# Performance work log

Hardware: AMD Instinct MI355X
Metric: run time of the kernel (lower is better)

## Reference

```python
import jax, jax.numpy as jnp
import numpy as np
import math

DIM_IN = 1024
DIM_HIDDEN = 512
NUM_SUBKEYS = 256
TOP_K = 32
NUM_HEADS = 4
BN_EPS = 1e-5


def setup_inputs() -> dict:
    key = jax.random.key(0)
    ks = jax.random.split(key, 6)
    std = 1.0 / math.sqrt(DIM_HIDDEN)
    x = jax.random.normal(ks[0], (4, 256, DIM_IN), dtype=jnp.float32)
    # nn.Linear weight: [out, in] = [dim_hidden*num_heads, dim_in]
    Wq = jax.random.normal(ks[1], (DIM_HIDDEN * NUM_HEADS, DIM_IN), dtype=jnp.float32) / math.sqrt(DIM_IN)
    bn_gamma = jnp.ones((DIM_HIDDEN * NUM_HEADS,), dtype=jnp.float32)
    bn_beta = jnp.zeros((DIM_HIDDEN * NUM_HEADS,), dtype=jnp.float32)
    subkey = DIM_HIDDEN // 2
    keyl = jax.random.uniform(ks[2], (NUM_HEADS, NUM_SUBKEYS, subkey), dtype=jnp.float32, minval=-std, maxval=std)
    keyr = jax.random.uniform(ks[3], (NUM_HEADS, NUM_SUBKEYS, subkey), dtype=jnp.float32, minval=-std, maxval=std)
    value_table = jax.random.normal(ks[4], (NUM_SUBKEYS * NUM_SUBKEYS, DIM_IN), dtype=jnp.float32)
    return {"x": x, "Wq": Wq, "bn_gamma": bn_gamma, "bn_beta": bn_beta,
            "keyl": keyl, "keyr": keyr, "value_table": value_table}


def reference(x, Wq, bn_gamma, bn_beta, keyl, keyr, value_table):
    b, c, _ = x.shape
    k = TOP_K
    subkey = DIM_HIDDEN // 2

    # QueryNetwork: linear (no bias) + BatchNorm1d (training-mode batch stats)
    q = jnp.einsum('bci,oi->bco', x, Wq)                      # [b, c, H*Dh]
    qf = q.reshape(-1, DIM_HIDDEN * NUM_HEADS)
    mean = jnp.mean(qf, axis=0)
    var = jnp.var(qf, axis=0)                                  # biased, as in torch BN forward
    qf = (qf - mean) * jax.lax.rsqrt(var + BN_EPS) * bn_gamma + bn_beta
    query = qf.reshape(b, c, NUM_HEADS, DIM_HIDDEN)

    # ProductKey: dual subkey scoring
    ql, qr = query[..., :subkey], query[..., subkey:]
    scorel = jnp.einsum('bcnq,nkq->bcnk', ql, keyl)            # [b,c,n,num_subkeys]
    scorer = jnp.einsum('bcnq,nkq->bcnk', qr, keyr)
    top_l, idx_l = jax.lax.top_k(scorel, k)                    # [b,c,n,k]
    top_r, idx_r = jax.lax.top_k(scorer, k)

    # Cartesian product of scores: s[i,j] = top_l[i] + top_r[j]
    product_scores = (top_l[..., :, None] + top_r[..., None, :]).reshape(b, c, NUM_HEADS, k * k)
    # NOTE: faithful to original code, idx_r is broadcast along the SAME (left)
    # axis as idx_l (original expands [...,k,1] -> [...,k,k] for both).
    pair_idx = idx_l * NUM_SUBKEYS + idx_r                     # [b,c,n,k]
    product_indices = jnp.broadcast_to(pair_idx[..., :, None], (b, c, NUM_HEADS, k, k)).reshape(b, c, NUM_HEADS, k * k)

    top_scores, top_pos = jax.lax.top_k(product_scores, k)     # [b,c,n,k]
    weights = jax.nn.softmax(top_scores, axis=-1)
    sel_idx = jnp.take_along_axis(product_indices, top_pos, axis=-1)  # [b,c,n,k]

    # Embedding gather + weighted sum over heads and k
    values = value_table[sel_idx]                              # [b,c,n,k,dim_in]
    out = jnp.einsum('bcnk,bcnkd->bcd', weights, values)
    return out
```

## Files before the change

### kernel.cpp

```cpp
#include <hip/hip_runtime.h>
#include <math.h>

#define N_TOK 1024
#define DIN   1024
#define DHID  2048
#define NSUB  256
#define SKDIM 256
#define NH    4
#define TOPK  32

#define TILE 64
#define BKQ  16

#define EPS_TIE  8e-7
#define EPS_PROD 1.2e-6
#define W_CAP    0.032f
#define SLOTS    72

__global__ __launch_bounds__(256) void gemm_q(const float* __restrict__ X,
                                              const float* __restrict__ W,
                                              double* __restrict__ Q) {
  __shared__ float As[BKQ][TILE + 4];
  __shared__ float Bs[BKQ][TILE + 4];
  const int tid = threadIdx.x;
  const int gm0 = blockIdx.y * TILE;
  const int gn0 = blockIdx.x * TILE;
  const int lr = tid >> 2;
  const int lc = (tid & 3) << 2;
  const int tx = tid & 15;
  const int ty = tid >> 4;
  double acc[4][4] = {};
  for (int k0 = 0; k0 < DIN; k0 += BKQ) {
    float4 av = *(const float4*)&X[(size_t)(gm0 + lr) * DIN + k0 + lc];
    float4 bv = *(const float4*)&W[(size_t)(gn0 + lr) * DIN + k0 + lc];
    __syncthreads();
    As[lc + 0][lr] = av.x; As[lc + 1][lr] = av.y; As[lc + 2][lr] = av.z; As[lc + 3][lr] = av.w;
    Bs[lc + 0][lr] = bv.x; Bs[lc + 1][lr] = bv.y; Bs[lc + 2][lr] = bv.z; Bs[lc + 3][lr] = bv.w;
    __syncthreads();
#pragma unroll
    for (int kk = 0; kk < BKQ; kk++) {
      float4 a = *(const float4*)&As[kk][tx << 2];
      float4 b = *(const float4*)&Bs[kk][ty << 2];
      double a0 = a.x, a1 = a.y, a2 = a.z, a3 = a.w;
      double b0 = b.x, b1 = b.y, b2 = b.z, b3 = b.w;
      acc[0][0] += a0 * b0; acc[0][1] += a0 * b1; acc[0][2] += a0 * b2; acc[0][3] += a0 * b3;
      acc[1][0] += a1 * b0; acc[1][1] += a1 * b1; acc[1][2] += a1 * b2; acc[1][3] += a1 * b3;
      acc[2][0] += a2 * b0; acc[2][1] += a2 * b1; acc[2][2] += a2 * b2; acc[2][3] += a2 * b3;
      acc[3][0] += a3 * b0; acc[3][1] += a3 * b1; acc[3][2] += a3 * b2; acc[3][3] += a3 * b3;
    }
  }
#pragma unroll
  for (int i = 0; i < 4; i++)
#pragma unroll
    for (int j = 0; j < 4; j++)
      Q[(size_t)(gm0 + (tx << 2) + i) * DHID + gn0 + (ty << 2) + j] = acc[i][j];
}

__global__ void bn_partial(const double* __restrict__ Q,
                           double* __restrict__ psum, double* __restrict__ psq) {
  const int col = blockIdx.x * 256 + threadIdx.x;
  const int rg = blockIdx.y;
  double s = 0.0, q2 = 0.0;
  for (int r = rg * 64; r < rg * 64 + 64; r++) {
    double v = Q[(size_t)r * DHID + col];
    s += v; q2 += v * v;
  }
  psum[rg * DHID + col] = s;
  psq[rg * DHID + col] = q2;
}

__global__ void bn_final(const double* __restrict__ psum, const double* __restrict__ psq,
                         double* __restrict__ mean, double* __restrict__ rstd) {
  const int col = blockIdx.x * 256 + threadIdx.x;
  double s = 0.0, q2 = 0.0;
  for (int rg = 0; rg < 16; rg++) { s += psum[rg * DHID + col]; q2 += psq[rg * DHID + col]; }
  double m = s * (1.0 / N_TOK);
  double var = q2 * (1.0 / N_TOK) - m * m;
  mean[col] = m;
  rstd[col] = 1.0 / sqrt(var + 1e-5);
}

__global__ __launch_bounds__(256) void scores_kernel(const double* __restrict__ Q,
    const double* __restrict__ mean, const double* __restrict__ rstd,
    const float* __restrict__ gamma, const float* __restrict__ beta,
    const float* __restrict__ keyl, const float* __restrict__ keyr,
    double* __restrict__ scorel, double* __restrict__ scorer) {
  __shared__ double As[BKQ][TILE + 2];
  __shared__ double Bs[BKQ][TILE + 2];
  const int tid = threadIdx.x;
  const int head = blockIdx.z >> 1;
  const int side = blockIdx.z & 1;
  const int base = head * 512 + side * 256;
  const float* __restrict__ key = side ? keyr : keyl;
  double* __restrict__ S = side ? scorer : scorel;
  const int gm0 = blockIdx.y * TILE;
  const int gn0 = blockIdx.x * TILE;
  const int lr = tid >> 2;
  const int lc = (tid & 3) << 2;
  const int tx = tid & 15;
  const int ty = tid >> 4;
  double acc[4][4] = {};
  for (int k0 = 0; k0 < SKDIM; k0 += BKQ) {
    const int c = base + k0 + lc;
    double qv[4], av[4];
#pragma unroll
    for (int u = 0; u < 4; u++) qv[u] = Q[(size_t)(gm0 + lr) * DHID + c + u];
#pragma unroll
    for (int u = 0; u < 4; u++)
      av[u] = (qv[u] - mean[c + u]) * rstd[c + u] * (double)gamma[c + u] + (double)beta[c + u];
    float4 bv = *(const float4*)&key[((size_t)(head * NSUB) + gn0 + lr) * SKDIM + k0 + lc];
    __syncthreads();
    As[lc + 0][lr] = av[0]; As[lc + 1][lr] = av[1]; As[lc + 2][lr] = av[2]; As[lc + 3][lr] = av[3];
    Bs[lc + 0][lr] = (double)bv.x; Bs[lc + 1][lr] = (double)bv.y;
    Bs[lc + 2][lr] = (double)bv.z; Bs[lc + 3][lr] = (double)bv.w;
    __syncthreads();
#pragma unroll
    for (int kk = 0; kk < BKQ; kk++) {
      double a0 = As[kk][(tx << 2) + 0], a1 = As[kk][(tx << 2) + 1];
      double a2 = As[kk][(tx << 2) + 2], a3 = As[kk][(tx << 2) + 3];
      double b0 = Bs[kk][(ty << 2) + 0], b1 = Bs[kk][(ty << 2) + 1];
      double b2 = Bs[kk][(ty << 2) + 2], b3 = Bs[kk][(ty << 2) + 3];
      acc[0][0] += a0 * b0; acc[0][1] += a0 * b1; acc[0][2] += a0 * b2; acc[0][3] += a0 * b3;
      acc[1][0] += a1 * b0; acc[1][1] += a1 * b1; acc[1][2] += a1 * b2; acc[1][3] += a1 * b3;
      acc[2][0] += a2 * b0; acc[2][1] += a2 * b1; acc[2][2] += a2 * b2; acc[2][3] += a2 * b3;
      acc[3][0] += a3 * b0; acc[3][1] += a3 * b1; acc[3][2] += a3 * b2; acc[3][3] += a3 * b3;
    }
  }
#pragma unroll
  for (int i = 0; i < 4; i++) {
    const int m = gm0 + (tx << 2) + i;
#pragma unroll
    for (int j = 0; j < 4; j++)
      S[((size_t)m * NH + head) * NSUB + gn0 + (ty << 2) + j] = acc[i][j];
  }
}

template<int NREG>
__device__ __forceinline__ void bitonic_wave_desc(double (&v)[NREG], int (&x)[NREG],
                                                  const int lane) {
  const int N = NREG * 64;
#pragma unroll
  for (int k = 2; k <= N; k <<= 1) {
#pragma unroll
    for (int j = k >> 1; j > 0; j >>= 1) {
      if (j >= 64) {
        const int jr = j >> 6;
#pragma unroll
        for (int r = 0; r < NREG; r++) {
          if ((r & jr) == 0) {
            const int r2 = r | jr;
            const int i = r * 64 + lane;
            const bool up = ((i & k) == 0);
            const bool af = (v[r] > v[r2]) || (v[r] == v[r2] && x[r] < x[r2]);
            if (up ? !af : af) {
              double tv = v[r]; v[r] = v[r2]; v[r2] = tv;
              int ti = x[r]; x[r] = x[r2]; x[r2] = ti;
            }
          }
        }
      } else {
#pragma unroll
        for (int r = 0; r < NREG; r++) {
          const double ov = __shfl_xor(v[r], j, 64);
          const int    oi = __shfl_xor(x[r], j, 64);
          const int i = r * 64 + lane;
          const bool up = ((i & k) == 0);
          const bool lower = ((lane & j) == 0);
          const double a = lower ? v[r] : ov; const int ia = lower ? x[r] : oi;
          const double b = lower ? ov : v[r]; const int ib = lower ? oi : x[r];
          const bool af = (a > b) || (a == b && ia < ib);
          if (up ? !af : af) { v[r] = ov; x[r] = oi; }
        }
      }
    }
  }
}

__global__ __launch_bounds__(256) void topk_kernel(const double* __restrict__ scorel,
                                                   const double* __restrict__ scorer,
                                                   float* __restrict__ wts,
                                                   int* __restrict__ sel) {
  const int token = blockIdx.x;
  const int tid = threadIdx.x;
  const int head = tid >> 6;
  const int lane = tid & 63;

  __shared__ double s_tlv[NH][33]; __shared__ int s_tli[NH][33];
  __shared__ double s_trv[NH][33]; __shared__ int s_tri[NH][33];
  __shared__ float  s_famw[NH][32];
  __shared__ int    s_nalt[NH];

  const double* sl = scorel + ((size_t)token * NH + head) * NSUB;
  const double* sr = scorer + ((size_t)token * NH + head) * NSUB;

  double v[4]; int x[4];
#pragma unroll
  for (int r = 0; r < 4; r++) { v[r] = sl[r * 64 + lane]; x[r] = r * 64 + lane; }
  bitonic_wave_desc<4>(v, x, lane);
  if (lane < 33) { s_tlv[head][lane] = v[0]; s_tli[head][lane] = x[0]; }

#pragma unroll
  for (int r = 0; r < 4; r++) { v[r] = sr[r * 64 + lane]; x[r] = r * 64 + lane; }
  bitonic_wave_desc<4>(v, x, lane);
  if (lane < 33) { s_trv[head][lane] = v[0]; s_tri[head][lane] = x[0]; }
  __syncthreads();

  double cv[2]; int cx[2];
#pragma unroll
  for (int r = 0; r < 2; r++) {
    const int t = r * 64 + lane;
    double val = -INFINITY; int packed = 0x7F000000 + t;
    if (t < 119) {
      int rem = t, i = 0;
      for (;;) {
        int c = 32 / (i + 1);
        if (rem < c) break;
        rem -= c; i++;
      }
      val = s_tlv[head][i] + s_trv[head][rem];
      packed = (((i << 5) | rem) << 16) | (s_tli[head][i] * NSUB + s_tri[head][i]);
    }
    cv[r] = val; cx[r] = packed;
  }
  bitonic_wave_desc<2>(cv, cx, lane);

  const double m = __shfl(cv[0], 0, 64);
  const double ex = (lane < TOPK) ? exp(cv[0] - m) : 0.0;
  double ssum = ex;
#pragma unroll
  for (int d = 1; d < 64; d <<= 1) ssum += __shfl_xor(ssum, d, 64);
  double w = ex / ssum;

  const double bv = __shfl(cv[0], TOPK, 64);
  const int    bid = __shfl(cx[0], TOPK, 64) & 0xFFFF;

  const size_t obase = ((size_t)token * NH + head) * SLOTS;

  if (lane < SLOTS - TOPK) { wts[obase + TOPK + lane] = 0.f; sel[obase + TOPK + lane] = 0; }
  if (lane < 32) s_famw[head][lane] = 0.f;
  if (lane == 0) s_nalt[head] = 0;
  __syncthreads();

  const int packed = cx[0];
  const int id = packed & 0xFFFF;
  const int pi = (packed >> 21) & 31;

  if (lane < TOPK) atomicAdd(&s_famw[head][pi], (float)w);
  __syncthreads();

  if (lane < TOPK) {
    int alts[5]; int na = 0;
    if (s_famw[head][pi] <= W_CAP) {
      if (s_tlv[head][pi] - s_tlv[head][pi + 1] < EPS_TIE) alts[na++] = s_tli[head][pi + 1] * NSUB + s_tri[head][pi];
      if (s_trv[head][pi] - s_trv[head][pi + 1] < EPS_TIE) alts[na++] = s_tli[head][pi] * NSUB + s_tri[head][pi + 1];
      if (pi > 0) {
        if (s_tlv[head][pi - 1] - s_tlv[head][pi] < EPS_TIE) alts[na++] = s_tli[head][pi - 1] * NSUB + s_tri[head][pi];
        if (s_trv[head][pi - 1] - s_trv[head][pi] < EPS_TIE) alts[na++] = s_tli[head][pi] * NSUB + s_tri[head][pi - 1];
      }
      if (lane == TOPK - 1) {
        const double g3 = cv[0] - bv;
        if (g3 < EPS_PROD && bid != id) alts[na++] = bid;
      }
    }

    if (na > 0) {
      int base = atomicAdd(&s_nalt[head], na);
      int avail = (SLOTS - TOPK) - base; if (avail < 0) avail = 0;
      int got = na < avail ? na : avail;
      if (got > 0) {
        float wa = (float)(0.5 * w / na);
        for (int t = 0; t < got; t++) {
          wts[obase + TOPK + base + t] = wa;
          sel[obase + TOPK + base + t] = alts[t];
        }
        w -= (double)wa * got;
      }
    }
    wts[obase + lane] = (float)w;
    sel[obase + lane] = id;
  }
}

__global__ __launch_bounds__(256) void gather_kernel(const float* __restrict__ wts,
                                                     const int* __restrict__ sel,
                                                     const float* __restrict__ VT,
                                                     float* __restrict__ out) {
  __shared__ float w_s[NH * SLOTS];
  __shared__ int   i_s[NH * SLOTS];
  const int token = blockIdx.x;
  const int tid = threadIdx.x;
  for (int p = tid; p < NH * SLOTS; p += 256) {
    w_s[p] = wts[(size_t)token * NH * SLOTS + p];
    i_s[p] = sel[(size_t)token * NH * SLOTS + p];
  }
  __syncthreads();
  const int d = tid << 2;
  float4 acc = make_float4(0.f, 0.f, 0.f, 0.f);
  for (int p = 0; p < NH * SLOTS; p++) {
    float w = w_s[p];
    if (w == 0.f) continue;
    float4 v = *(const float4*)&VT[(size_t)i_s[p] * DIN + d];
    acc.x += w * v.x; acc.y += w * v.y; acc.z += w * v.z; acc.w += w * v.w;
  }
  *(float4*)&out[(size_t)token * DIN + d] = acc;
}

extern "C" void kernel_launch(void* const* d_in, const int* in_sizes, int n_in,
                              void* d_out, int out_size, void* d_ws, size_t ws_size,
                              hipStream_t stream) {
  const float* x     = (const float*)d_in[0];
  const float* Wq    = (const float*)d_in[1];
  const float* gamma = (const float*)d_in[2];
  const float* beta  = (const float*)d_in[3];
  const float* keyl  = (const float*)d_in[4];
  const float* keyr  = (const float*)d_in[5];
  const float* vt    = (const float*)d_in[6];
  float* out = (float*)d_out;

  double* wsd = (double*)d_ws;
  double* qd     = wsd;
  double* psum   = wsd + 2097152;
  double* psq    = wsd + 2129920;
  double* meand  = wsd + 2162688;
  double* rstdd  = wsd + 2164736;
  double* scl    = wsd + 2166784;
  double* scr    = wsd + 3215360;
  float*  wts    = (float*)(wsd + 4263936);
  int*    sel    = (int*)(wts + 294912);

  gemm_q<<<dim3(32, 16), 256, 0, stream>>>(x, Wq, qd);
  bn_partial<<<dim3(8, 16), 256, 0, stream>>>(qd, psum, psq);
  bn_final<<<8, 256, 0, stream>>>(psum, psq, meand, rstdd);
  scores_kernel<<<dim3(4, 16, 8), 256, 0, stream>>>(qd, meand, rstdd, gamma, beta,
                                                    keyl, keyr, scl, scr);
  topk_kernel<<<N_TOK, 256, 0, stream>>>(scl, scr, wts, sel);
  gather_kernel<<<N_TOK, 256, 0, stream>>>(wts, sel, vt, out);
}
```

Baseline: 611.4 us.

## Use FP64 MFMA matrix instructions for the query projection GEMM

Replaces the scalar double-precision FMA inner loop of the query GEMM with 16x16x4 FP64 MFMA instructions. Each wave computes a 32x32 subtile, and the shared tiles are now stored as doubles. The output layout of the MFMA accumulator is found at runtime with extra index-probing MFMAs, which adds a few syncs and LDS writes at the end. The aim is to cut the FP64 ALU cost of the projection, which is likely the dominant stage.

```diff
diff --git a/kernel.cpp b/kernel.cpp
--- a/kernel.cpp
+++ b/kernel.cpp
@@ -17,43 +17,101 @@
 #define W_CAP    0.032f
 #define SLOTS    72
 
+typedef double d4 __attribute__((ext_vector_type(4)));
+
 __global__ __launch_bounds__(256) void gemm_q(const float* __restrict__ X,
                                               const float* __restrict__ W,
                                               double* __restrict__ Q) {
-  __shared__ float As[BKQ][TILE + 4];
-  __shared__ float Bs[BKQ][TILE + 4];
+  __shared__ double As[BKQ][TILE + 2];
+  __shared__ double Bs[BKQ][TILE + 2];
   const int tid = threadIdx.x;
   const int gm0 = blockIdx.y * TILE;
   const int gn0 = blockIdx.x * TILE;
   const int lr = tid >> 2;
   const int lc = (tid & 3) << 2;
-  const int tx = tid & 15;
-  const int ty = tid >> 4;
-  double acc[4][4] = {};
+  const int wave = tid >> 6;
+  const int lane = tid & 63;
+  const int wr0 = (wave >> 1) * 32;
+  const int wc0 = (wave & 1) * 32;
+  const int fr = lane & 15;
+  const int fk = lane >> 4;
+
+  d4 acc[2][2];
+#pragma unroll
+  for (int i = 0; i < 2; i++)
+#pragma unroll
+    for (int j = 0; j < 2; j++)
+      acc[i][j] = (d4){0.0, 0.0, 0.0, 0.0};
+
   for (int k0 = 0; k0 < DIN; k0 += BKQ) {
     float4 av = *(const float4*)&X[(size_t)(gm0 + lr) * DIN + k0 + lc];
     float4 bv = *(const float4*)&W[(size_t)(gn0 + lr) * DIN + k0 + lc];
     __syncthreads();
-    As[lc + 0][lr] = av.x; As[lc + 1][lr] = av.y; As[lc + 2][lr] = av.z; As[lc + 3][lr] = av.w;
-    Bs[lc + 0][lr] = bv.x; Bs[lc + 1][lr] = bv.y; Bs[lc + 2][lr] = bv.z; Bs[lc + 3][lr] = bv.w;
+    As[lc + 0][lr] = (double)av.x; As[lc + 1][lr] = (double)av.y;
+    As[lc + 2][lr] = (double)av.z; As[lc + 3][lr] = (double)av.w;
+    Bs[lc + 0][lr] = (double)bv.x; Bs[lc + 1][lr] = (double)bv.y;
+    Bs[lc + 2][lr] = (double)bv.z; Bs[lc + 3][lr] = (double)bv.w;
     __syncthreads();
 #pragma unroll
-    for (int kk = 0; kk < BKQ; kk++) {
-      float4 a = *(const float4*)&As[kk][tx << 2];
-      float4 b = *(const float4*)&Bs[kk][ty << 2];
-      double a0 = a.x, a1 = a.y, a2 = a.z, a3 = a.w;
-      double b0 = b.x, b1 = b.y, b2 = b.z, b3 = b.w;
-      acc[0][0] += a0 * b0; acc[0][1] += a0 * b1; acc[0][2] += a0 * b2; acc[0][3] += a0 * b3;
-      acc[1][0] += a1 * b0; acc[1][1] += a1 * b1; acc[1][2] += a1 * b2; acc[1][3] += a1 * b3;
-      acc[2][0] += a2 * b0; acc[2][1] += a2 * b1; acc[2][2] += a2 * b2; acc[2][3] += a2 * b3;
-      acc[3][0] += a3 * b0; acc[3][1] += a3 * b1; acc[3][2] += a3 * b2; acc[3][3] += a3 * b3;
-    }
-  }
-#pragma unroll
-  for (int i = 0; i < 4; i++)
-#pragma unroll
-    for (int j = 0; j < 4; j++)
-      Q[(size_t)(gm0 + (tx << 2) + i) * DHID + gn0 + (ty << 2) + j] = acc[i][j];
+    for (int k4 = 0; k4 < BKQ; k4 += 4) {
+      const double a0 = As[k4 + fk][wr0 + fr];
+      const double a1 = As[k4 + fk][wr0 + 16 + fr];
+      const double b0 = Bs[k4 + fk][wc0 + fr];
+      const double b1 = Bs[k4 + fk][wc0 + 16 + fr];
+      acc[0][0] = __builtin_amdgcn_mfma_f64_16x16x4f64(a0, b0, acc[0][0], 0, 0, 0);
+      acc[0][1] = __builtin_amdgcn_mfma_f64_16x16x4f64(a0, b1, acc[0][1], 0, 0, 0);
+      acc[1][0] = __builtin_amdgcn_mfma_f64_16x16x4f64(a1, b0, acc[1][0], 0, 0, 0);
+      acc[1][1] = __builtin_amdgcn_mfma_f64_16x16x4f64(a1, b1, acc[1][1], 0, 0, 0);
+    }
+  }
+
+  const d4 zero4 = (d4){0.0, 0.0, 0.0, 0.0};
+  d4 drow0, drow1, dcol0, dcol1;
+  __syncthreads();
+#pragma unroll
+  for (int u = 0; u < 4; u++) {
+    As[lc + u][lr] = ((lc + u) == 0) ? (double)lr : 0.0;
+    Bs[lc + u][lr] = ((lc + u) == 0) ? 1.0 : 0.0;
+  }
+  __syncthreads();
+  {
+    const double ar0 = As[fk][wr0 + fr];
+    const double ar1 = As[fk][wr0 + 16 + fr];
+    const double bo  = Bs[fk][wc0 + fr];
+    drow0 = __builtin_amdgcn_mfma_f64_16x16x4f64(ar0, bo, zero4, 0, 0, 0);
+    drow1 = __builtin_amdgcn_mfma_f64_16x16x4f64(ar1, bo, zero4, 0, 0, 0);
+  }
+  __syncthreads();
+#pragma unroll
+  for (int u = 0; u < 4; u++) {
+    As[lc + u][lr] = ((lc + u) == 0) ? 1.0 : 0.0;
+    Bs[lc + u][lr] = ((lc + u) == 0) ? (double)lr : 0.0;
+  }
+  __syncthreads();
+  {
+    const double ao  = As[fk][wr0 + fr];
+    const double bc0 = Bs[fk][wc0 + fr];
+    const double bc1 = Bs[fk][wc0 + 16 + fr];
+    dcol0 = __builtin_amdgcn_mfma_f64_16x16x4f64(ao, bc0, zero4, 0, 0, 0);
+    dcol1 = __builtin_amdgcn_mfma_f64_16x16x4f64(ao, bc1, zero4, 0, 0, 0);
+  }
+
+#pragma unroll
+  for (int ti = 0; ti < 2; ti++) {
+#pragma unroll
+    for (int tj = 0; tj < 2; tj++) {
+#pragma unroll
+      for (int g = 0; g < 4; g++) {
+        const double drv = ti ? drow1[g] : drow0[g];
+        const double dcv = tj ? dcol1[g] : dcol0[g];
+        int r = (int)(drv + 0.5);
+        int c = (int)(dcv + 0.5);
+        if (r < 0 || r >= TILE) r = wr0 + ti * 16 + fk * 4 + g;
+        if (c < 0 || c >= TILE) c = wc0 + tj * 16 + fr;
+        Q[(size_t)(gm0 + r) * DHID + gn0 + c] = acc[ti][tj][g];
+      }
+    }
+  }
 }
 
 __global__ void bn_partial(const double* __restrict__ Q,
```

Result: faster. 575.3 us (-5.9%).
